# Kernel tuning notes

Measured on AMD Instinct MI355X. Metric: run time of the kernel, lower is better.

## Reference

```python
import jax, jax.numpy as jnp
import numpy as np

B, LC, LQ, D = 16, 1024, 128, 512


def setup_inputs() -> dict:
    key = jax.random.key(0)
    k1, k2, k3, k4, k5 = jax.random.split(key, 5)
    return {
        "C": jax.random.normal(k1, (B, LC, D), dtype=jnp.float32),
        "Q": jax.random.normal(k2, (B, LQ, D), dtype=jnp.float32),
        "Cmask": jax.random.randint(k3, (B, LC), 0, 2, dtype=jnp.int32),
        "Qmask": jax.random.randint(k4, (B, LQ), 0, 2, dtype=jnp.int32),
        "w_sim": jax.random.normal(k5, (3 * D,), dtype=jnp.float32) * (1.0 / np.sqrt(3 * D)),
    }


def reference(C, Q, Cmask, Qmask, w_sim):
    d = C.shape[-1]
    # Decompose Linear(3d -> 1) on cat([C_rep, Q_rep, C*Q]) into three dot products:
    # S[b,i,j] = C[b,i].w1 + Q[b,j].w2 + (C[b,i]*Q[b,j]).w3
    w1, w2, w3 = w_sim[:d], w_sim[d:2 * d], w_sim[2 * d:]
    s_c = C @ w1                                    # (B, Lc)
    s_q = Q @ w2                                    # (B, Lq)
    s_cq = jnp.einsum('bid,bjd->bij', C * w3, Q)    # (B, Lc, Lq)
    S = s_c[:, :, None] + s_q[:, None, :] + s_cq    # (B, Lc, Lq)

    NEG = jnp.asarray(-1e10, S.dtype)
    S1 = jax.nn.softmax(jnp.where(Qmask[:, None, :] != 0, NEG, S), axis=2)  # over question
    S2 = jax.nn.softmax(jnp.where(Cmask[:, :, None] != 0, NEG, S), axis=1)  # over context

    A = jnp.einsum('bij,bjd->bid', S1, Q)                       # (B, Lc, d)
    # bmm(bmm(S1, S2^T), C) == S1 @ (S2^T @ C) (associativity, avoids Lc x Lc)
    S2tC = jnp.einsum('bij,bid->bjd', S2, C)                    # (B, Lq, d)
    Bv = jnp.einsum('bij,bjd->bid', S1, S2tC)                   # (B, Lc, d)

    # dropout treated as identity (eval / p-effective 0) for the reference
    return jnp.concatenate([C, A, C * A, C * Bv], axis=2)       # (B, Lc, 4d)
```

## Files before the change

kernel.cpp:

```cpp
#include <hip/hip_runtime.h>
#include <hip/hip_bf16.h>
#include <math.h>

#define NB 16
#define NLC 1024
#define NLQ 128
#define ND 512
#define NEGV (-1.0e10f)

typedef __attribute__((ext_vector_type(8))) short bf16x8f;
typedef __attribute__((ext_vector_type(4))) float f32x4a;

__device__ inline unsigned short f2bf(float f) {
    unsigned u = __float_as_uint(f);
    unsigned r = (u + 0x7fffu + ((u >> 16) & 1u)) >> 16;
    return (unsigned short)r;
}

__device__ inline int xcd_swz(int bid, int nwg) {
    int chunk = nwg >> 3;
    return (bid & 7) * chunk + (bid >> 3);
}

__global__ __launch_bounds__(512) void k_prep2(const float* __restrict__ C,
                                               const float* __restrict__ Q,
                                               const float* __restrict__ w,
                                               unsigned short* __restrict__ Cw3,
                                               unsigned short* __restrict__ Ct,
                                               unsigned short* __restrict__ Qb,
                                               unsigned short* __restrict__ Qt,
                                               float* __restrict__ scp,
                                               float* __restrict__ sqp) {
    __shared__ float T[64][65];
    int x = blockIdx.x, t = threadIdx.x;
    const float* src; const float* wdot; const float* wmul;
    unsigned short* rout; unsigned short* tout; float* sdst;
    int rows;
    if (x < 512) {
        int b = x >> 5, rt = (x >> 1) & 15, dh = x & 1;
        src = C + ((size_t)b * NLC + rt * 64) * ND + dh * 256;
        wdot = w + dh * 256;
        wmul = w + 2 * ND + dh * 256;
        rout = Cw3 + ((size_t)b * NLC + rt * 64) * ND + dh * 256;
        tout = Ct + ((size_t)b * ND + dh * 256) * NLC + rt * 64;
        sdst = scp + dh * (NB * NLC) + b * NLC + rt * 64;
        rows = NLC;
    } else {
        int xq = x - 512;
        int b = xq >> 2, rt = (xq >> 1) & 1, dh = xq & 1;
        src = Q + ((size_t)b * NLQ + rt * 64) * ND + dh * 256;
        wdot = w + ND + dh * 256;
        wmul = nullptr;
        rout = Qb + ((size_t)b * NLQ + rt * 64) * ND + dh * 256;
        tout = Qt + ((size_t)b * ND + dh * 256) * NLQ + rt * 64;
        sdst = sqp + dh * (NB * NLQ) + b * NLQ + rt * 64;
        rows = NLQ;
    }
    int r = t >> 3;
    int s8 = (t & 7) * 8;
    float dacc = 0.f;
    for (int c = 0; c < 4; ++c) {
        int dbase = c * 64 + s8;
        float4 v0 = *(const float4*)&src[(size_t)r * ND + dbase];
        float4 v1 = *(const float4*)&src[(size_t)r * ND + dbase + 4];
        float4 wd0 = *(const float4*)&wdot[dbase];
        float4 wd1 = *(const float4*)&wdot[dbase + 4];
        dacc += v0.x * wd0.x + v0.y * wd0.y + v0.z * wd0.z + v0.w * wd0.w;
        dacc += v1.x * wd1.x + v1.y * wd1.y + v1.z * wd1.z + v1.w * wd1.w;
        float f8[8] = {v0.x, v0.y, v0.z, v0.w, v1.x, v1.y, v1.z, v1.w};
        unsigned short o[8];
        if (wmul) {
            float4 w30 = *(const float4*)&wmul[dbase];
            float4 w31 = *(const float4*)&wmul[dbase + 4];
            float m8[8] = {w30.x, w30.y, w30.z, w30.w, w31.x, w31.y, w31.z, w31.w};
#pragma unroll
            for (int e = 0; e < 8; ++e) o[e] = f2bf(f8[e] * m8[e]);
        } else {
#pragma unroll
            for (int e = 0; e < 8; ++e) o[e] = f2bf(f8[e]);
        }
        *(int4*)&rout[(size_t)r * ND + dbase] = *(int4*)o;
#pragma unroll
        for (int e = 0; e < 8; ++e) T[r][s8 + e] = f8[e];
        __syncthreads();
        {
            int dd = t >> 3, seg = (t & 7) * 8;
            unsigned short o16[8];
#pragma unroll
            for (int e = 0; e < 8; ++e) o16[e] = f2bf(T[seg + e][dd]);
            *(int4*)&tout[(size_t)(c * 64 + dd) * rows + seg] = *(int4*)o16;
        }
        __syncthreads();
    }
    dacc += __shfl_xor(dacc, 1, 64);
    dacc += __shfl_xor(dacc, 2, 64);
    dacc += __shfl_xor(dacc, 4, 64);
    if ((t & 7) == 0) sdst[r] = dacc;
}

__global__ __launch_bounds__(256) void k_S(const unsigned short* __restrict__ Cw3,
                                           const unsigned short* __restrict__ Qb,
                                           const float* __restrict__ scp,
                                           const float* __restrict__ sqp,
                                           const int* __restrict__ Qmask,
                                           const int* __restrict__ Cmask,
                                           unsigned short* __restrict__ P1,
                                           unsigned short* __restrict__ Eb,
                                           float* __restrict__ colm,
                                           float* __restrict__ cols) {
    __shared__ __align__(16) char lds[49152];
    int lg = xcd_swz(blockIdx.x, 256);
    int b = lg >> 4, it = lg & 15, i0 = it * 64;
    int t = threadIdx.x, lane = t & 63, wv = t >> 6;
    int g = lane >> 4, r16 = lane & 15;
    const unsigned short* Asrc = Cw3 + ((size_t)b * NLC + i0) * ND;
    const unsigned short* Bsrc = Qb + (size_t)b * NLQ * ND;
    f32x4a zero = {0.f, 0.f, 0.f, 0.f};
    f32x4a acc[8];
#pragma unroll
    for (int nf = 0; nf < 8; ++nf) acc[nf] = zero;

    for (int kk = 0; kk < 4; ++kk) {
#pragma unroll
        for (int p = 0; p < 4; ++p) {
            int u = t + p * 256;
            int i = u >> 4, db = u & 15;
            int4 v = *(const int4*)(Asrc + (size_t)i * ND + kk * 128 + db * 8);
            *(int4*)(lds + i * 256 + ((db * 16) ^ ((i & 7) << 4))) = v;
        }
#pragma unroll
        for (int p = 0; p < 8; ++p) {
            int u = t + p * 256;
            int j = u >> 4, db = u & 15;
            int4 v = *(const int4*)(Bsrc + (size_t)j * ND + kk * 128 + db * 8);
            *(int4*)(lds + 16384 + j * 256 + ((db * 16) ^ ((j & 7) << 4))) = v;
        }
        __syncthreads();
#pragma unroll
        for (int ks = 0; ks < 4; ++ks) {
            int inner = ks * 64 + g * 16;
            bf16x8f a = *(const bf16x8f*)(lds + (16 * wv + r16) * 256 + (inner ^ ((r16 & 7) << 4)));
#pragma unroll
            for (int nf = 0; nf < 8; ++nf) {
                bf16x8f bq = *(const bf16x8f*)(lds + 16384 + (16 * nf + r16) * 256 + (inner ^ ((r16 & 7) << 4)));
                acc[nf] = __builtin_amdgcn_mfma_f32_16x16x32_bf16(a, bq, acc[nf], 0, 0, 0);
            }
        }
        __syncthreads();
    }

    const float* scp0 = scp + b * NLC + i0;
    const float* scp1 = scp + NB * NLC + b * NLC + i0;
    const float* sqp0 = sqp + b * NLQ;
    const float* sqp1 = sqp + NB * NLQ + b * NLQ;
    const int* qm = Qmask + b * NLQ;
    const int* cmb = Cmask + b * NLC;
    float sv[8][4];
    float scr[4];
#pragma unroll
    for (int reg = 0; reg < 4; ++reg) {
        int il = 16 * wv + 4 * g + reg;
        scr[reg] = scp0[il] + scp1[il];
    }
    int qmv[8];
#pragma unroll
    for (int nf = 0; nf < 8; ++nf) {
        int jl = 16 * nf + r16;
        qmv[nf] = qm[jl];
        float sqv = sqp0[jl] + sqp1[jl];
#pragma unroll
        for (int reg = 0; reg < 4; ++reg) sv[nf][reg] = acc[nf][reg] + scr[reg] + sqv;
    }

    unsigned short* P1p = P1 + ((size_t)b * NLC + i0) * NLQ;
#pragma unroll
    for (int reg = 0; reg < 4; ++reg) {
        float m = -INFINITY;
#pragma unroll
        for (int nf = 0; nf < 8; ++nf) m = fmaxf(m, qmv[nf] ? NEGV : sv[nf][reg]);
#pragma unroll
        for (int off = 8; off >= 1; off >>= 1) m = fmaxf(m, __shfl_xor(m, off, 64));
        float pv[8], s = 0.f;
#pragma unroll
        for (int nf = 0; nf < 8; ++nf) {
            pv[nf] = __expf((qmv[nf] ? NEGV : sv[nf][reg]) - m);
            s += pv[nf];
        }
#pragma unroll
        for (int off = 8; off >= 1; off >>= 1) s += __shfl_xor(s, off, 64);
        float rsi = 1.0f / s;
        int i = 16 * wv + 4 * g + reg;
#pragma unroll
        for (int nf = 0; nf < 8; ++nf)
            P1p[(size_t)i * NLQ + 16 * nf + r16] = f2bf(pv[nf] * rsi);
    }

    int cmv[4];
#pragma unroll
    for (int reg = 0; reg < 4; ++reg) cmv[reg] = cmb[i0 + 16 * wv + 4 * g + reg];
    float vm2[8][4];
#pragma unroll
    for (int nf = 0; nf < 8; ++nf)
#pragma unroll
        for (int reg = 0; reg < 4; ++reg) vm2[nf][reg] = cmv[reg] ? NEGV : sv[nf][reg];

    float* cpm = (float*)(lds + 20480);
    float* cps = (float*)(lds + 22528);
    float* mtl = (float*)(lds + 24576);
    float cm8[8], cs8[8];
#pragma unroll
    for (int nf = 0; nf < 8; ++nf) {
        float m = vm2[nf][0];
#pragma unroll
        for (int reg = 1; reg < 4; ++reg) m = fmaxf(m, vm2[nf][reg]);
        float s = 0.f;
#pragma unroll
        for (int reg = 0; reg < 4; ++reg) s += __expf(vm2[nf][reg] - m);
#pragma unroll
        for (int off = 16; off <= 32; off <<= 1) {
            float mo = __shfl_xor(m, off, 64);
            float so = __shfl_xor(s, off, 64);
            float mn = fmaxf(m, mo);
            s = s * __expf(m - mn) + so * __expf(mo - mn);
            m = mn;
        }
        cm8[nf] = m; cs8[nf] = s;
    }
    if (g == 0) {
#pragma unroll
        for (int nf = 0; nf < 8; ++nf) {
            cpm[(wv * 8 + nf) * 16 + r16] = cm8[nf];
            cps[(wv * 8 + nf) * 16 + r16] = cs8[nf];
        }
    }
    __syncthreads();
    if (t < 128) {
        int j = t, nf = j >> 4, rr = j & 15;
        float M = cpm[(0 * 8 + nf) * 16 + rr];
        float S = cps[(0 * 8 + nf) * 16 + rr];
#pragma unroll
        for (int w2 = 1; w2 < 4; ++w2) {
            float mo = cpm[(w2 * 8 + nf) * 16 + rr];
            float so = cps[(w2 * 8 + nf) * 16 + rr];
            float mn = fmaxf(M, mo);
            S = S * __expf(M - mn) + so * __expf(mo - mn);
            M = mn;
        }
        colm[((size_t)b * 16 + it) * NLQ + j] = M;
        cols[((size_t)b * 16 + it) * NLQ + j] = S;
        mtl[j] = M;
    }
    __syncthreads();

    unsigned short* ex = (unsigned short*)lds;
#pragma unroll
    for (int nf = 0; nf < 8; ++nf) {
        float mj = mtl[16 * nf + r16];
        unsigned short e4[4];
#pragma unroll
        for (int reg = 0; reg < 4; ++reg) e4[reg] = f2bf(__expf(vm2[nf][reg] - mj));
        *(uint2*)&ex[(16 * nf + r16) * 80 + 16 * wv + 4 * g] = *(uint2*)e4;
    }
    __syncthreads();
    {
        int j = t >> 1, half = t & 1;
        unsigned short* Ep = Eb + ((size_t)b * NLQ + j) * NLC + i0 + half * 32;
#pragma unroll
        for (int c = 0; c < 4; ++c)
            *(int4*)&Ep[c * 8] = *(int4*)&ex[j * 80 + half * 32 + c * 8];
    }
}

__global__ __launch_bounds__(256) void k_s2tc(const unsigned short* __restrict__ Eb,
                                              const unsigned short* __restrict__ Ct,
                                              const float* __restrict__ colm,
                                              const float* __restrict__ cols,
                                              unsigned short* __restrict__ Vt) {
    __shared__ __align__(16) char lds[23552];
    int lg = xcd_swz(blockIdx.x, 128);
    int b = lg >> 3, dt = lg & 7;
    int t = threadIdx.x, lane = t & 63, wv = t >> 6, g = lane >> 4, r16 = lane & 15;
    float* fb = (float*)lds;

    if (t < 128) {
        int j = t;
        const float* cmp = colm + (size_t)b * 16 * NLQ + j;
        const float* csp = cols + (size_t)b * 16 * NLQ + j;
        float M = -INFINITY;
#pragma unroll
        for (int p = 0; p < 16; ++p) M = fmaxf(M, cmp[p * NLQ]);
        float S = 0.f;
#pragma unroll
        for (int p = 0; p < 16; ++p) S += csp[p * NLQ] * __expf(cmp[p * NLQ] - M);
        float inv = 1.0f / S;
#pragma unroll
        for (int p = 0; p < 16; ++p) fb[p * NLQ + j] = __expf(cmp[p * NLQ] - M) * inv;
    }

    const unsigned short* Ebb = Eb + (size_t)b * NLQ * NLC;
    const unsigned short* Ctb = Ct + ((size_t)b * ND + dt * 64) * NLC;
    int ja0 = t >> 2, ca0 = (t & 3) * 8;
    int ja1 = (t + 256) >> 2, ca1 = ((t + 256) & 3) * 8;
    int db0 = t >> 2, cb0 = (t & 3) * 8;

    f32x4a zero = {0.f, 0.f, 0.f, 0.f};
    f32x4a acc2[2][4], V[2][4];
#pragma unroll
    for (int mf = 0; mf < 2; ++mf)
#pragma unroll
        for (int nf = 0; nf < 4; ++nf) { acc2[mf][nf] = zero; V[mf][nf] = zero; }

    int4 ra0 = *(const int4*)(Ebb + (size_t)ja0 * NLC + ca0);
    int4 ra1 = *(const int4*)(Ebb + (size_t)ja1 * NLC + ca1);
    int4 rb  = *(const int4*)(Ctb + (size_t)db0 * NLC + cb0);
    __syncthreads();

    for (int ib = 0; ib < NLC; ib += 32) {
        *(int4*)(lds + 8192 + (ja0 * 40 + ca0) * 2) = ra0;
        *(int4*)(lds + 8192 + (ja1 * 40 + ca1) * 2) = ra1;
        *(int4*)(lds + 18432 + (db0 * 40 + cb0) * 2) = rb;
        __syncthreads();
        if (ib + 32 < NLC) {
            ra0 = *(const int4*)(Ebb + (size_t)ja0 * NLC + ib + 32 + ca0);
            ra1 = *(const int4*)(Ebb + (size_t)ja1 * NLC + ib + 32 + ca1);
            rb  = *(const int4*)(Ctb + (size_t)db0 * NLC + ib + 32 + cb0);
        }
#pragma unroll
        for (int mf = 0; mf < 2; ++mf) {
            bf16x8f a = *(const bf16x8f*)(lds + 8192 + ((32 * wv + 16 * mf + r16) * 40 + g * 8) * 2);
#pragma unroll
            for (int nf = 0; nf < 4; ++nf) {
                bf16x8f bb = *(const bf16x8f*)(lds + 18432 + ((16 * nf + r16) * 40 + g * 8) * 2);
                acc2[mf][nf] = __builtin_amdgcn_mfma_f32_16x16x32_bf16(a, bb, acc2[mf][nf], 0, 0, 0);
            }
        }
        __syncthreads();
        if (ib & 32) {
            int itg = ib >> 6;
#pragma unroll
            for (int mf = 0; mf < 2; ++mf) {
                f32x4a f4 = *(const f32x4a*)(lds + (itg * NLQ + 32 * wv + 16 * mf + 4 * g) * 4);
#pragma unroll
                for (int nf = 0; nf < 4; ++nf) {
#pragma unroll
                    for (int reg = 0; reg < 4; ++reg)
                        V[mf][nf][reg] += f4[reg] * acc2[mf][nf][reg];
                    acc2[mf][nf] = zero;
                }
            }
        }
    }
    unsigned short* vb = Vt + ((size_t)b * ND + dt * 64) * NLQ;
#pragma unroll
    for (int mf = 0; mf < 2; ++mf)
#pragma unroll
        for (int nf = 0; nf < 4; ++nf) {
            unsigned short o[4];
#pragma unroll
            for (int reg = 0; reg < 4; ++reg) o[reg] = f2bf(V[mf][nf][reg]);
            *(uint2*)&vb[(size_t)(16 * nf + r16) * NLQ + 32 * wv + 16 * mf + 4 * g] = *(uint2*)o;
        }
}

__global__ __launch_bounds__(256) void k_out(const unsigned short* __restrict__ P1,
                                             const unsigned short* __restrict__ Qt,
                                             const unsigned short* __restrict__ Vt,
                                             const float* __restrict__ C,
                                             float* __restrict__ Out) {
    __shared__ __align__(16) char lds[49152];
    int lg = xcd_swz(blockIdx.x, 2048);
    int b = lg >> 7, rem = lg & 127, it = rem >> 3, dt = rem & 7;
    int i0 = it * 64, d0 = dt * 64;
    int t = threadIdx.x, lane = t & 63, wv = t >> 6, g = lane >> 4, r16 = lane & 15;

    const float* Cb = C + ((size_t)b * NLC + i0) * ND + d0;
    f32x4a cpre[4];
#pragma unroll
    for (int p = 0; p < 4; ++p) {
        int u = t + p * 256;
        cpre[p] = *(const f32x4a*)&Cb[(size_t)(u >> 4) * ND + (u & 15) * 4];
    }

    const unsigned short* P1b = P1 + ((size_t)b * NLC + i0) * NLQ;
    const unsigned short* Qtb = Qt + ((size_t)b * ND + d0) * NLQ;
    const unsigned short* Vtb = Vt + ((size_t)b * ND + d0) * NLQ;
#pragma unroll
    for (int p = 0; p < 4; ++p) {
        int u = t + p * 256;
        int r = u >> 4, c = u & 15;
        int swz = (c * 16) ^ ((r & 7) << 4);
        *(int4*)(lds + r * 256 + swz) = *(const int4*)(P1b + (size_t)r * NLQ + c * 8);
        *(int4*)(lds + 16384 + r * 256 + swz) = *(const int4*)(Qtb + (size_t)r * NLQ + c * 8);
        *(int4*)(lds + 32768 + r * 256 + swz) = *(const int4*)(Vtb + (size_t)r * NLQ + c * 8);
    }
    __syncthreads();
    f32x4a zero = {0.f, 0.f, 0.f, 0.f};
    f32x4a accA[4], accB[4];
#pragma unroll
    for (int nf = 0; nf < 4; ++nf) { accA[nf] = zero; accB[nf] = zero; }
#pragma unroll
    for (int ks = 0; ks < 4; ++ks) {
        int inner = ks * 64 + g * 16;
        bf16x8f a = *(const bf16x8f*)(lds + (16 * wv + r16) * 256 + (inner ^ ((r16 & 7) << 4)));
#pragma unroll
        for (int nf = 0; nf < 4; ++nf) {
            int ro = (16 * nf + r16) * 256 + (inner ^ ((r16 & 7) << 4));
            bf16x8f q = *(const bf16x8f*)(lds + 16384 + ro);
            accA[nf] = __builtin_amdgcn_mfma_f32_16x16x32_bf16(a, q, accA[nf], 0, 0, 0);
            bf16x8f vv = *(const bf16x8f*)(lds + 32768 + ro);
            accB[nf] = __builtin_amdgcn_mfma_f32_16x16x32_bf16(a, vv, accB[nf], 0, 0, 0);
        }
    }
    __syncthreads();

    float* At = (float*)lds;
    float* Bt = (float*)(lds + 17408);
#pragma unroll
    for (int nf = 0; nf < 4; ++nf) {
        int dloc = 16 * nf + r16;
#pragma unroll
        for (int reg = 0; reg < 4; ++reg) {
            int iloc = 16 * wv + 4 * g + reg;
            At[iloc * 68 + dloc] = accA[nf][reg];
            Bt[iloc * 68 + dloc] = accB[nf][reg];
        }
    }
    __syncthreads();

    float* Ob = Out + ((size_t)b * NLC + i0) * (4 * ND);
#pragma unroll
    for (int p = 0; p < 4; ++p) {
        int u = t + p * 256;
        int row = u >> 4, c4 = (u & 15) * 4;
        f32x4a cv = cpre[p];
        f32x4a av = *(const f32x4a*)&At[row * 68 + c4];
        f32x4a bv = *(const f32x4a*)&Bt[row * 68 + c4];
        f32x4a ca = cv * av;
        f32x4a cb = cv * bv;
        float* orow = Ob + (size_t)row * (4 * ND);
        *(f32x4a*)&orow[d0 + c4] = cv;
        *(f32x4a*)&orow[ND + d0 + c4] = av;
        *(f32x4a*)&orow[2 * ND + d0 + c4] = ca;
        *(f32x4a*)&orow[3 * ND + d0 + c4] = cb;
    }
}

extern "C" void kernel_launch(void* const* d_in, const int* in_sizes, int n_in,
                              void* d_out, int out_size, void* d_ws, size_t ws_size,
                              hipStream_t stream) {
    const float* C = (const float*)d_in[0];
    const float* Q = (const float*)d_in[1];
    const int* Cmask = (const int*)d_in[2];
    const int* Qmask = (const int*)d_in[3];
    const float* w = (const float*)d_in[4];
    float* out = (float*)d_out;

    char* ob = (char*)d_out;
    unsigned short* Cw3 = (unsigned short*)(ob + 0);
    unsigned short* Ct  = (unsigned short*)(ob + 16777216);
    unsigned short* Eb  = (unsigned short*)(ob + 33554432);
    unsigned short* Qb  = (unsigned short*)(ob + 37748736);
    float*          colm = (float*)(ob + 39845888);
    float*          colsv = (float*)(ob + 39976960);
    float*          scp  = (float*)(ob + 40108032);
    float*          sqp  = (float*)(ob + 40239104);

    char* wb = (char*)d_ws;
    unsigned short* P1 = (unsigned short*)(wb + 73728);
    unsigned short* Qt = (unsigned short*)(wb + 4268032);
    unsigned short* Vt = (unsigned short*)(wb + 6365184);

    k_prep2<<<dim3(576), dim3(512), 0, stream>>>(C, Q, w, Cw3, Ct, Qb, Qt, scp, sqp);
    k_S<<<dim3(256), dim3(256), 0, stream>>>(Cw3, Qb, scp, sqp, Qmask, Cmask, P1, Eb, colm, colsv);
    k_s2tc<<<dim3(128), dim3(256), 0, stream>>>(Eb, Ct, colm, colsv, Vt);
    k_out<<<dim3(2048), dim3(256), 0, stream>>>(P1, Qt, Vt, C, out);
}
```

Measured before the change: 76.80 us.

## Split S2^T C reduction over context into two halves, sum partials in output kernel

k_s2tc now launches 256 blocks instead of 128, each reducing over half of the context dimension and writing a separate partial Vt slice. k_out loads both partial V slices and accumulates two MFMA passes, so the sum happens implicitly through linearity. This is meant to fill more CUs in the under-occupied s2tc kernel. In exchange, k_out does extra LDS traffic, extra MFMA work and an additional barrier pair, and the Vt workspace doubles.

Result: slower. 80.82 us (+5.2%).

```diff
diff --git a/kernel.cpp b/kernel.cpp
--- a/kernel.cpp
+++ b/kernel.cpp
@@ -277,8 +277,8 @@
                                               const float* __restrict__ cols,
                                               unsigned short* __restrict__ Vt) {
     __shared__ __align__(16) char lds[23552];
-    int lg = xcd_swz(blockIdx.x, 128);
-    int b = lg >> 3, dt = lg & 7;
+    int lg = xcd_swz(blockIdx.x, 256);
+    int b = lg >> 4, dt = (lg >> 1) & 7, ih = lg & 1;
     int t = threadIdx.x, lane = t & 63, wv = t >> 6, g = lane >> 4, r16 = lane & 15;
     float* fb = (float*)lds;
 
@@ -310,17 +310,18 @@
 #pragma unroll
         for (int nf = 0; nf < 4; ++nf) { acc2[mf][nf] = zero; V[mf][nf] = zero; }
 
-    int4 ra0 = *(const int4*)(Ebb + (size_t)ja0 * NLC + ca0);
-    int4 ra1 = *(const int4*)(Ebb + (size_t)ja1 * NLC + ca1);
-    int4 rb  = *(const int4*)(Ctb + (size_t)db0 * NLC + cb0);
-    __syncthreads();
-
-    for (int ib = 0; ib < NLC; ib += 32) {
+    int ibeg = ih * 512, iend = ibeg + 512;
+    int4 ra0 = *(const int4*)(Ebb + (size_t)ja0 * NLC + ibeg + ca0);
+    int4 ra1 = *(const int4*)(Ebb + (size_t)ja1 * NLC + ibeg + ca1);
+    int4 rb  = *(const int4*)(Ctb + (size_t)db0 * NLC + ibeg + cb0);
+    __syncthreads();
+
+    for (int ib = ibeg; ib < iend; ib += 32) {
         *(int4*)(lds + 8192 + (ja0 * 40 + ca0) * 2) = ra0;
         *(int4*)(lds + 8192 + (ja1 * 40 + ca1) * 2) = ra1;
         *(int4*)(lds + 18432 + (db0 * 40 + cb0) * 2) = rb;
         __syncthreads();
-        if (ib + 32 < NLC) {
+        if (ib + 32 < iend) {
             ra0 = *(const int4*)(Ebb + (size_t)ja0 * NLC + ib + 32 + ca0);
             ra1 = *(const int4*)(Ebb + (size_t)ja1 * NLC + ib + 32 + ca1);
             rb  = *(const int4*)(Ctb + (size_t)db0 * NLC + ib + 32 + cb0);
@@ -350,7 +351,7 @@
             }
         }
     }
-    unsigned short* vb = Vt + ((size_t)b * ND + dt * 64) * NLQ;
+    unsigned short* vb = Vt + ((size_t)(ih * NB + b) * ND + dt * 64) * NLQ;
 #pragma unroll
     for (int mf = 0; mf < 2; ++mf)
 #pragma unroll
@@ -383,7 +384,8 @@
 
     const unsigned short* P1b = P1 + ((size_t)b * NLC + i0) * NLQ;
     const unsigned short* Qtb = Qt + ((size_t)b * ND + d0) * NLQ;
-    const unsigned short* Vtb = Vt + ((size_t)b * ND + d0) * NLQ;
+    const unsigned short* Vtb0 = Vt + ((size_t)b * ND + d0) * NLQ;
+    const unsigned short* Vtb1 = Vt + ((size_t)(NB + b) * ND + d0) * NLQ;
 #pragma unroll
     for (int p = 0; p < 4; ++p) {
         int u = t + p * 256;
@@ -391,7 +393,13 @@
         int swz = (c * 16) ^ ((r & 7) << 4);
         *(int4*)(lds + r * 256 + swz) = *(const int4*)(P1b + (size_t)r * NLQ + c * 8);
         *(int4*)(lds + 16384 + r * 256 + swz) = *(const int4*)(Qtb + (size_t)r * NLQ + c * 8);
-        *(int4*)(lds + 32768 + r * 256 + swz) = *(const int4*)(Vtb + (size_t)r * NLQ + c * 8);
+        *(int4*)(lds + 32768 + r * 256 + swz) = *(const int4*)(Vtb0 + (size_t)r * NLQ + c * 8);
+    }
+    int4 rv1[4];
+#pragma unroll
+    for (int p = 0; p < 4; ++p) {
+        int u = t + p * 256;
+        rv1[p] = *(const int4*)(Vtb1 + (size_t)(u >> 4) * NLQ + (u & 15) * 8);
     }
     __syncthreads();
     f32x4a zero = {0.f, 0.f, 0.f, 0.f};
@@ -407,6 +415,26 @@
             int ro = (16 * nf + r16) * 256 + (inner ^ ((r16 & 7) << 4));
             bf16x8f q = *(const bf16x8f*)(lds + 16384 + ro);
             accA[nf] = __builtin_amdgcn_mfma_f32_16x16x32_bf16(a, q, accA[nf], 0, 0, 0);
+            bf16x8f vv = *(const bf16x8f*)(lds + 32768 + ro);
+            accB[nf] = __builtin_amdgcn_mfma_f32_16x16x32_bf16(a, vv, accB[nf], 0, 0, 0);
+        }
+    }
+    __syncthreads();
+#pragma unroll
+    for (int p = 0; p < 4; ++p) {
+        int u = t + p * 256;
+        int r = u >> 4, c = u & 15;
+        int swz = (c * 16) ^ ((r & 7) << 4);
+        *(int4*)(lds + 32768 + r * 256 + swz) = rv1[p];
+    }
+    __syncthreads();
+#pragma unroll
+    for (int ks = 0; ks < 4; ++ks) {
+        int inner = ks * 64 + g * 16;
+        bf16x8f a = *(const bf16x8f*)(lds + (16 * wv + r16) * 256 + (inner ^ ((r16 & 7) << 4)));
+#pragma unroll
+        for (int nf = 0; nf < 4; ++nf) {
+            int ro = (16 * nf + r16) * 256 + (inner ^ ((r16 & 7) << 4));
             bf16x8f vv = *(const bf16x8f*)(lds + 32768 + ro);
             accB[nf] = __builtin_amdgcn_mfma_f32_16x16x32_bf16(a, vv, accB[nf], 0, 0, 0);
         }
@@ -472,6 +500,6 @@
 
     k_prep2<<<dim3(576), dim3(512), 0, stream>>>(C, Q, w, Cw3, Ct, Qb, Qt, scp, sqp);
     k_S<<<dim3(256), dim3(256), 0, stream>>>(Cw3, Qb, scp, sqp, Qmask, Cmask, P1, Eb, colm, colsv);
-    k_s2tc<<<dim3(128), dim3(256), 0, stream>>>(Eb, Ct, colm, colsv, Vt);
+    k_s2tc<<<dim3(256), dim3(256), 0, stream>>>(Eb, Ct, colm, colsv, Vt);
     k_out<<<dim3(2048), dim3(256), 0, stream>>>(P1, Qt, Vt, C, out);
 }
```
